# Performance work log

Hardware: AMD Instinct MI355X
Metric: run time of the kernel (lower is better)

The kernel has to match this reference:

```python
import jax, jax.numpy as jnp
import numpy as np

K = 6

def _diag_indices(H, W):
    # stable argsort of anti-diagonal index i+j over row-major flattening
    i = np.arange(H)[:, None]
    j = np.arange(W)[None, :]
    order = np.argsort((i + j).ravel(), kind='stable')
    return order, np.argsort(order, kind='stable')

def _selective_scan(u, delta, A, Bs, Cs, D, delta_bias):
    # u, delta: (B,K,D,L); A: (K,D,N); Bs,Cs: (B,K,N,L); D,delta_bias: (K,D)
    delta = jax.nn.softplus(delta + delta_bias[None, :, :, None])
    dA = jnp.exp(jnp.einsum('bkdl,kdn->lbkdn', delta, A))          # (L,B,K,D,N)
    dBu = jnp.einsum('bkdl,bknl,bkdl->lbkdn', delta, Bs, u)         # (L,B,K,D,N)
    Cl = jnp.moveaxis(Cs, -1, 0)                                    # (L,B,K,N)
    x0 = jnp.zeros(dA.shape[1:], dA.dtype)
    def step(x, inp):
        dA_t, dBu_t, C_t = inp
        x = dA_t * x + dBu_t
        y = jnp.einsum('bkdn,bkn->bkd', x, C_t)
        return x, y
    _, ys = jax.lax.scan(step, x0, (dA, dBu, Cl))
    y = jnp.moveaxis(ys, 0, -1)                                     # (B,K,D,L)
    return y + u * D[None, :, :, None]

def reference(x, W_in, conv_w, conv_b, x_proj_w, dt_w, dt_b, A_logs, Ds, ln_g, ln_b, W_out):
    B, H, W, C = x.shape
    L = H * W
    di = dt_w.shape[1]
    dt_rank = dt_w.shape[2]
    N = A_logs.shape[1]
    # in_proj (no bias) and split
    xz = jnp.einsum('bhwc,oc->bhwo', x, W_in)
    xx, z = jnp.split(xz, 2, axis=-1)
    # depthwise conv 3x3, SAME padding, + bias, SiLU
    xc = jnp.transpose(xx, (0, 3, 1, 2))                            # (B,di,H,W)
    xc = jax.lax.conv_general_dilated(xc, conv_w, (1, 1), 'SAME',
            feature_group_count=di, dimension_numbers=('NCHW', 'OIHW', 'NCHW'))
    xc = jax.nn.silu(xc + conv_b[None, :, None, None])
    # build 6 scan orderings
    x_flat = xc.reshape(B, di, L)
    x_t = jnp.transpose(xc, (0, 1, 3, 2)).reshape(B, di, L)
    x_hwwh = jnp.stack([x_flat, x_t], axis=1)                       # (B,2,di,L)
    xs4 = jnp.concatenate([x_hwwh, x_hwwh[..., ::-1]], axis=1)      # (B,4,di,L)
    x_invhh = jnp.flip(xc, axis=-1).reshape(B, di, L)               # flip W only
    x_hh = jnp.stack([x_flat, x_invhh], axis=1)                     # (B,2,di,L)
    diag_idx, rev_idx = _diag_indices(H, W)
    xs = jnp.concatenate([xs4, x_hh[..., diag_idx]], axis=1)        # (B,6,di,L)
    # projections
    x_dbl = jnp.einsum('bkdl,kcd->bkcl', xs, x_proj_w)
    dts, Bs, Cs = jnp.split(x_dbl, [dt_rank, dt_rank + N], axis=2)
    dts = jnp.einsum('bkrl,kdr->bkdl', dts, dt_w)
    A = -jnp.exp(A_logs).reshape(K, di, N)
    out_y = _selective_scan(xs, dts, A, Bs, Cs, Ds.reshape(K, di), dt_b)
    # undo the 6 orderings
    inv_y = out_y[:, 2:4][..., ::-1]
    wh_y = jnp.transpose(out_y[:, 1].reshape(B, di, W, H), (0, 1, 3, 2)).reshape(B, di, L)
    invwh_y = jnp.transpose(inv_y[:, 1].reshape(B, di, W, H), (0, 1, 3, 2)).reshape(B, di, L)
    transhh = out_y[:, 4:6][..., rev_idx]
    invhh = transhh[:, 1][..., ::-1]
    y = out_y[:, 0] + inv_y[:, 0] + wh_y + invwh_y + transhh[:, 0] + invhh  # (B,di,L)
    y = jnp.transpose(y, (0, 2, 1)).reshape(B, H, W, di)
    # LayerNorm (eps=1e-5)
    mu = y.mean(-1, keepdims=True)
    var = ((y - mu) ** 2).mean(-1, keepdims=True)
    y = (y - mu) * jax.lax.rsqrt(var + 1e-5) * ln_g + ln_b
    y = y * jax.nn.silu(z)
    return jnp.einsum('bhwd,od->bhwo', y, W_out)

def setup_inputs():
    key = jax.random.key(0)
    ks = jax.random.split(key, 8)
    d_model, di, N, dt_rank = 64, 128, 16, 4
    x = jax.random.normal(ks[0], (1, 64, 64, d_model), jnp.float32)
    W_in = jax.random.normal(ks[1], (2 * di, d_model), jnp.float32) * d_model ** -0.5
    conv_w = jax.random.normal(ks[2], (di, 1, 3, 3), jnp.float32) / 3.0
    conv_b = jnp.zeros((di,), jnp.float32)
    x_proj_w = jax.random.normal(ks[3], (K, dt_rank + 2 * N, di), jnp.float32) * di ** -0.5
    s = dt_rank ** -0.5
    dt_w = jax.random.uniform(ks[4], (K, di, dt_rank), jnp.float32, -s, s)
    dt = jnp.exp(jax.random.uniform(ks[5], (K, di), jnp.float32)
                 * (np.log(0.1) - np.log(0.001)) + np.log(0.001))
    dt = jnp.clip(dt, 1e-4)
    dt_b = dt + jnp.log(-jnp.expm1(-dt))
    A_logs = jnp.log(jnp.tile(jnp.arange(1, N + 1, dtype=jnp.float32)[None, :], (K * di, 1)))
    Ds = jnp.ones((K * di,), jnp.float32)
    ln_g = jnp.ones((di,), jnp.float32)
    ln_b = jnp.zeros((di,), jnp.float32)
    W_out = jax.random.normal(ks[6], (d_model, di), jnp.float32) * di ** -0.5
    return {"x": x, "W_in": W_in, "conv_w": conv_w, "conv_b": conv_b,
            "x_proj_w": x_proj_w, "dt_w": dt_w, "dt_b": dt_b, "A_logs": A_logs,
            "Ds": Ds, "ln_g": ln_g, "ln_b": ln_b, "W_out": W_out}
```

## Files before the change

kernel.cpp:

```cpp
#include <hip/hip_runtime.h>
#include <math.h>

#define L    4096
#define DI   128
#define NS   16
#define KK   6
#define DTR  4
#define CM   64
#define NC   256
#define CH   (L/NC)

__device__ __forceinline__ float softplus_f(float x){
    return x > 20.f ? x : __logf(1.f + __expf(x));
}
__device__ __forceinline__ float silu_f(float x){
    return x / (1.f + __expf(-x));
}

__device__ __forceinline__ int rankp(int p){
    int h = p >> 6, w = p & 63, s = h + w;
    int imin = s > 63 ? s - 63 : 0;
    int off = (s < 64) ? (s*(s+1))/2 : 4096 - ((127-s)*(128-s))/2;
    return off + (h - imin);
}

__device__ __forceinline__ int perm_in(int k, int l, const int* __restrict__ diag){
    switch(k){
        case 0: return l;
        case 1: return ((l&63)<<6) | (l>>6);
        case 2: return (L-1) - l;
        case 3: { int m = (L-1)-l; return ((m&63)<<6) | (m>>6); }
        case 4: return diag[l];
        default: return diag[l] ^ 63;
    }
}

__global__ void k_diag(int* __restrict__ diag_idx){
    int p = blockIdx.x*256 + threadIdx.x;
    if(p >= L) return;
    diag_idx[rankp(p)] = p;
}

__global__ __launch_bounds__(256) void k_inproj(const float* __restrict__ x,
                                                const float* __restrict__ W_in,
                                                float* __restrict__ xx_t,
                                                float* __restrict__ sz){
    int pb = blockIdx.x * 16;
    int o  = threadIdx.x;
    __shared__ float xr[16][CM];
    ((float4*)&xr[0][0])[o] = ((const float4*)(x + (size_t)pb*CM))[o];
    float4 w[16];
    const float4* wrow = (const float4*)(W_in + (size_t)o*CM);
    #pragma unroll
    for(int q=0;q<16;q++) w[q] = wrow[q];
    __syncthreads();
    #pragma unroll
    for(int pi=0; pi<16; pi++){
        float acc = 0.f;
        const float4* xv4 = (const float4*)&xr[pi][0];
        #pragma unroll
        for(int q=0;q<16;q++){
            float4 xv = xv4[q];
            acc += w[q].x*xv.x + w[q].y*xv.y + w[q].z*xv.z + w[q].w*xv.w;
        }
        int p = pb + pi;
        if(o < DI) xx_t[(size_t)p*DI + o] = acc;
        else       sz[(size_t)p*DI + (o-DI)] = silu_f(acc);
    }
}

__global__ __launch_bounds__(256) void k_conv(const float* __restrict__ xx_t,
                                              const float* __restrict__ cw,
                                              const float* __restrict__ cb,
                                              float* __restrict__ xc_t){
    int idx = blockIdx.x*256 + threadIdx.x;
    int d = idx & 127, p = idx >> 7;
    int h = p >> 6, w = p & 63;
    float acc = cb[d];
    #pragma unroll
    for(int dh=-1; dh<=1; dh++){
        int hh = h+dh; if(hh < 0 || hh >= 64) continue;
        #pragma unroll
        for(int dw=-1; dw<=1; dw++){
            int ww = w+dw; if(ww < 0 || ww >= 64) continue;
            acc += cw[d*9 + (dh+1)*3+(dw+1)] * xx_t[(size_t)(hh*64+ww)*DI + d];
        }
    }
    xc_t[idx] = silu_f(acc);
}

#define XT_S 132
__global__ __launch_bounds__(256) void k_proj(const float* __restrict__ xc_t,
                                              const float* __restrict__ xpw,
                                              const int* __restrict__ diag,
                                              float* __restrict__ dts,
                                              float* __restrict__ BT,
                                              float* __restrict__ CT){
    int k  = blockIdx.x >> 6;
    int l0 = (blockIdx.x & 63) * 64;
    int t  = threadIdx.x;
    __shared__ float xt[64*XT_S];
    #pragma unroll
    for(int q=0;q<8;q++){
        int lin = q*256 + t;
        int row = lin >> 5, col4 = lin & 31;
        int p = perm_in(k, l0+row, diag);
        float4 v = ((const float4*)(xc_t + (size_t)p*DI))[col4];
        *((float4*)(xt + row*XT_S + col4*4)) = v;
    }
    __syncthreads();
    int l = t & 63, c0 = (t>>6)*9;
    const float* xr = xt + l*XT_S;
    float acc[9];
    #pragma unroll
    for(int j=0;j<9;j++) acc[j] = 0.f;
    const float4* wbase = (const float4*)(xpw + (size_t)k*36*DI);
    for(int dd4=0; dd4<32; dd4++){
        float4 xv = *((const float4*)(xr + dd4*4));
        #pragma unroll
        for(int j=0;j<9;j++){
            float4 wv = wbase[(c0+j)*32 + dd4];
            acc[j] += wv.x*xv.x + wv.y*xv.y + wv.z*xv.z + wv.w*xv.w;
        }
    }
    #pragma unroll
    for(int j=0;j<9;j++){
        int c = c0 + j;
        if(c < 4)        dts[((size_t)k*4 + c)*L + l0 + l] = acc[j];
        else if(c < 20)  BT[((size_t)k*L + l0 + l)*NS + (c-4)]  = acc[j];
        else             CT[((size_t)k*L + l0 + l)*NS + (c-20)] = acc[j];
    }
}

__global__ __launch_bounds__(128) void k_scan1(const float* __restrict__ xc_t,
                                               const float* __restrict__ dts,
                                               const float* __restrict__ BT,
                                               const float* __restrict__ dtw,
                                               const float* __restrict__ dtb,
                                               const float* __restrict__ A_logs,
                                               const int* __restrict__ diag,
                                               float* __restrict__ apb,
                                               float* __restrict__ xlb){
    int bk = blockIdx.x;
    int k = bk >> 8, cc = bk & (NC-1);
    int d = threadIdx.x;
    int l0 = cc*CH;

    __shared__ float Bt[CH*NS];
    __shared__ float dtt[4*CH];
    __shared__ int   pt[CH];

    if(d < 64) ((float4*)Bt)[d] = ((const float4*)(BT + ((size_t)k*L + l0)*NS))[d];
    else { int j = d-64; int r = j>>4, i = j&15;
           dtt[j] = dts[((size_t)k*4 + r)*L + l0 + i]; }
    if(d < CH) pt[d] = perm_in(k, l0+d, diag);
    __syncthreads();

    float4 w4 = ((const float4*)dtw)[(size_t)k*DI + d];
    float  bb = dtb[k*DI + d];
    float A[NS];
    {
        const float4* ar = (const float4*)(A_logs + ((size_t)k*DI + d)*NS);
        #pragma unroll
        for(int q=0;q<4;q++){
            float4 a4 = ar[q];
            A[q*4+0] = -__expf(a4.x); A[q*4+1] = -__expf(a4.y);
            A[q*4+2] = -__expf(a4.z); A[q*4+3] = -__expf(a4.w);
        }
    }
    float x[NS], ap[NS];
    #pragma unroll
    for(int n=0;n<NS;n++){ x[n] = 0.f; ap[n] = 1.f; }

    float u_nxt = xc_t[(size_t)pt[0]*DI + d];
    #pragma unroll
    for(int i=0;i<CH;i++){
        float u = u_nxt;
        if(i+1 < CH) u_nxt = xc_t[(size_t)pt[i+1]*DI + d];
        float dv = bb + w4.x*dtt[i] + w4.y*dtt[CH+i] + w4.z*dtt[2*CH+i] + w4.w*dtt[3*CH+i];
        float delta = softplus_f(dv);
        float du = delta*u;
        const float* Bi = Bt + i*NS;
        #pragma unroll
        for(int n=0;n<NS;n++){
            float da = __expf(delta*A[n]);
            x[n] = da*x[n] + du*Bi[n];
            ap[n] *= da;
        }
    }
    float* apd = apb + ((size_t)bk*DI + d)*NS;
    float* xld = xlb + ((size_t)bk*DI + d)*NS;
    #pragma unroll
    for(int q=0;q<4;q++){
        ((float4*)apd)[q] = make_float4(ap[q*4],ap[q*4+1],ap[q*4+2],ap[q*4+3]);
        ((float4*)xld)[q] = make_float4(x[q*4], x[q*4+1], x[q*4+2], x[q*4+3]);
    }
}

__global__ __launch_bounds__(256) void k_comb(float* __restrict__ apb,
                                              const float* __restrict__ xlb){
    int tid = blockIdx.x*256 + threadIdx.x;
    int k = tid >> 11, rem = tid & 2047;
    size_t base = (size_t)k*NC*2048 + rem;
    float run = 0.f;
    float a[8], xl[8];
    #pragma unroll
    for(int q=0;q<8;q++){ a[q] = apb[base + (size_t)q*2048]; xl[q] = xlb[base + (size_t)q*2048]; }
    for(int b=0; b<NC/8; b++){
        float a2[8], x2[8];
        if(b+1 < NC/8){
            #pragma unroll
            for(int q=0;q<8;q++){
                size_t off = base + (size_t)((b+1)*8+q)*2048;
                a2[q] = apb[off]; x2[q] = xlb[off];
            }
        }
        #pragma unroll
        for(int q=0;q<8;q++){
            size_t off = base + (size_t)(b*8+q)*2048;
            apb[off] = run;
            run = a[q]*run + xl[q];
        }
        #pragma unroll
        for(int q=0;q<8;q++){ a[q] = a2[q]; xl[q] = x2[q]; }
    }
}

__global__ __launch_bounds__(128) void k_scan2(const float* __restrict__ xc_t,
                                               const float* __restrict__ dts,
                                               const float* __restrict__ BT,
                                               const float* __restrict__ CT,
                                               const float* __restrict__ dtw,
                                               const float* __restrict__ dtb,
                                               const float* __restrict__ A_logs,
                                               const float* __restrict__ Dsv,
                                               const int* __restrict__ diag,
                                               const float* __restrict__ inib,
                                               float* __restrict__ yk){
    int bk = blockIdx.x;
    int k = bk >> 8, cc = bk & (NC-1);
    int d = threadIdx.x;
    int l0 = cc*CH;

    __shared__ float Bt[CH*NS];
    __shared__ float Ct[CH*NS];
    __shared__ float dtt[4*CH];
    __shared__ int   pt[CH];

    if(d < 64){
        ((float4*)Bt)[d] = ((const float4*)(BT + ((size_t)k*L + l0)*NS))[d];
        int r = d>>4, i = d&15;
        dtt[d] = dts[((size_t)k*4 + r)*L + l0 + i];
    } else {
        ((float4*)Ct)[d-64] = ((const float4*)(CT + ((size_t)k*L + l0)*NS))[d-64];
    }
    if(d < CH) pt[d] = perm_in(k, l0+d, diag);
    __syncthreads();

    float4 w4 = ((const float4*)dtw)[(size_t)k*DI + d];
    float  bb = dtb[k*DI + d];
    float  Dv = Dsv[k*DI + d];
    float A[NS];
    {
        const float4* ar = (const float4*)(A_logs + ((size_t)k*DI + d)*NS);
        #pragma unroll
        for(int q=0;q<4;q++){
            float4 a4 = ar[q];
            A[q*4+0] = -__expf(a4.x); A[q*4+1] = -__expf(a4.y);
            A[q*4+2] = -__expf(a4.z); A[q*4+3] = -__expf(a4.w);
        }
    }
    float x[NS];
    {
        const float4* ir = (const float4*)(inib + ((size_t)bk*DI + d)*NS);
        #pragma unroll
        for(int q=0;q<4;q++){
            float4 v = ir[q];
            x[q*4+0]=v.x; x[q*4+1]=v.y; x[q*4+2]=v.z; x[q*4+3]=v.w;
        }
    }

    float u_nxt = xc_t[(size_t)pt[0]*DI + d];
    #pragma unroll
    for(int i=0;i<CH;i++){
        float u = u_nxt;
        if(i+1 < CH) u_nxt = xc_t[(size_t)pt[i+1]*DI + d];
        float dv = bb + w4.x*dtt[i] + w4.y*dtt[CH+i] + w4.z*dtt[2*CH+i] + w4.w*dtt[3*CH+i];
        float delta = softplus_f(dv);
        float du = delta*u;
        const float* Bi = Bt + i*NS;
        const float* Ci = Ct + i*NS;
        float y = 0.f;
        #pragma unroll
        for(int n=0;n<NS;n++){
            float da = __expf(delta*A[n]);
            x[n] = da*x[n] + du*Bi[n];
            y += x[n]*Ci[n];
        }
        yk[((size_t)k*L + l0 + i)*DI + d] = y + u*Dv;
    }
}

__global__ __launch_bounds__(128) void k_out(const float* __restrict__ yk,
                                             const float* __restrict__ sz,
                                             const float* __restrict__ ln_g,
                                             const float* __restrict__ ln_b,
                                             const float* __restrict__ W_out,
                                             float* __restrict__ out){
    int pb = blockIdx.x*8;
    int d = threadIdx.x;
    __shared__ float ms[8][DI];
    __shared__ float red[8][2][2];
    float g = ln_g[d], bc = ln_b[d];
    float yv[8];
    #pragma unroll
    for(int pi=0;pi<8;pi++){
        int p = pb+pi;
        int tp = ((p&63)<<6) | (p>>6);
        float y;
        y  = yk[((size_t)0*L + p)*DI + d];
        y += yk[((size_t)1*L + tp)*DI + d];
        y += yk[((size_t)2*L + (L-1-p))*DI + d];
        y += yk[((size_t)3*L + (L-1-tp))*DI + d];
        y += yk[((size_t)4*L + rankp(p))*DI + d];
        y += yk[((size_t)5*L + rankp(L-1-p))*DI + d];
        yv[pi] = y;
        float s1 = y, s2 = y*y;
        #pragma unroll
        for(int m=1;m<64;m<<=1){ s1 += __shfl_xor(s1,m,64); s2 += __shfl_xor(s2,m,64); }
        if((d&63)==0){ red[pi][d>>6][0] = s1; red[pi][d>>6][1] = s2; }
    }
    __syncthreads();
    #pragma unroll
    for(int pi=0;pi<8;pi++){
        float mu  = (red[pi][0][0]+red[pi][1][0]) * (1.f/DI);
        float var = (red[pi][0][1]+red[pi][1][1]) * (1.f/DI) - mu*mu;
        float yh = (yv[pi]-mu)*rsqrtf(var+1e-5f)*g + bc;
        ms[pi][d] = yh * sz[(size_t)(pb+pi)*DI + d];
    }
    __syncthreads();
    int o = d & 63, hf = d >> 6;
    float4 w[32];
    const float4* wr4 = (const float4*)(W_out + (size_t)o*DI);
    #pragma unroll
    for(int q=0;q<32;q++) w[q] = wr4[q];
    for(int pi=hf; pi<8; pi+=2){
        float acc = 0.f;
        const float4* mr = (const float4*)ms[pi];
        #pragma unroll
        for(int q=0;q<32;q++){
            float4 xv = mr[q];
            acc += w[q].x*xv.x + w[q].y*xv.y + w[q].z*xv.z + w[q].w*xv.w;
        }
        out[(size_t)(pb+pi)*CM + o] = acc;
    }
}

extern "C" void kernel_launch(void* const* d_in, const int* in_sizes, int n_in,
                              void* d_out, int out_size, void* d_ws, size_t ws_size,
                              hipStream_t stream) {
    const float* x      = (const float*)d_in[0];
    const float* W_in   = (const float*)d_in[1];
    const float* conv_w = (const float*)d_in[2];
    const float* conv_b = (const float*)d_in[3];
    const float* xpw    = (const float*)d_in[4];
    const float* dtw    = (const float*)d_in[5];
    const float* dtb    = (const float*)d_in[6];
    const float* A_logs = (const float*)d_in[7];
    const float* Dsv    = (const float*)d_in[8];
    const float* ln_g   = (const float*)d_in[9];
    const float* ln_b   = (const float*)d_in[10];
    const float* W_out  = (const float*)d_in[11];
    float* out = (float*)d_out;

    float* ws = (float*)d_ws;
    float* xx_t = ws;
    float* sz   = xx_t + (size_t)L*DI;
    float* xc_t = sz   + (size_t)L*DI;
    float* dts  = xc_t + (size_t)L*DI;
    float* BT   = dts  + (size_t)KK*4*L;
    float* CT   = BT   + (size_t)KK*L*NS;
    float* apb  = CT   + (size_t)KK*L*NS;
    float* xlb  = apb  + (size_t)KK*NC*DI*NS;
    float* yk   = xlb  + (size_t)KK*NC*DI*NS;
    int*   diag = (int*)(yk + (size_t)KK*L*DI);

    k_diag  <<<L/256, 256, 0, stream>>>(diag);
    k_inproj<<<L/16, 256, 0, stream>>>(x, W_in, xx_t, sz);
    k_conv  <<<(L*DI)/256, 256, 0, stream>>>(xx_t, conv_w, conv_b, xc_t);
    k_proj  <<<KK*64, 256, 0, stream>>>(xc_t, xpw, diag, dts, BT, CT);
    k_scan1 <<<KK*NC, 128, 0, stream>>>(xc_t, dts, BT, dtw, dtb, A_logs, diag, apb, xlb);
    k_comb  <<<KK*DI*NS/256, 256, 0, stream>>>(apb, xlb);
    k_scan2 <<<KK*NC, 128, 0, stream>>>(xc_t, dts, BT, CT, dtw, dtb, A_logs, Dsv, diag, apb, yk);
    k_out   <<<L/8, 128, 0, stream>>>(yk, sz, ln_g, ln_b, W_out, out);
}
```

Measured before the change: 195.1 us.

## Fuse pipeline into front kernel plus cooperative persistent scan kernel

Merges in_proj and the depthwise conv into one tiled kernel with halo recompute, and computes the diagonal permutation analytically instead of through a lookup table. The x_proj is fused into the first scan pass, which now emits a local y and cumulative delta. A correction pass adds the carried-in state as C·exp(A·S)·x0, so the second full recurrence over the chunk is no longer run. The remaining stages run in one cooperative persistent kernel with grid syncs, falling back to separate launches. This trades launch overhead and extra passes for grid-sync costs, larger workspace traffic and halo recomputation.

Measured after the change: 220.0 us. +12.8%, slower.

```diff
diff --git a/kernel.cpp b/kernel.cpp
--- a/kernel.cpp
+++ b/kernel.cpp
@@ -1,14 +1,18 @@
 #include <hip/hip_runtime.h>
+#include <hip/hip_cooperative_groups.h>
 #include <math.h>
+
+namespace cg = cooperative_groups;
 
 #define L    4096
 #define DI   128
 #define NS   16
 #define KK   6
-#define DTR  4
 #define CM   64
 #define NC   256
-#define CH   (L/NC)
+#define CH   16
+#define NU   (KK*NC)
+#define SHSZ 2688
 
 __device__ __forceinline__ float softplus_f(float x){
     return x > 20.f ? x : __logf(1.f + __expf(x));
@@ -23,141 +27,160 @@
     int off = (s < 64) ? (s*(s+1))/2 : 4096 - ((127-s)*(128-s))/2;
     return off + (h - imin);
 }
-
-__device__ __forceinline__ int perm_in(int k, int l, const int* __restrict__ diag){
+__device__ __forceinline__ int diag_pix(int l){
+    if(l < 2080){
+        int s = (int)((sqrtf(8.f*(float)l + 1.f) - 1.f)*0.5f);
+        if((s+1)*(s+2)/2 <= l) s++;
+        else if(s*(s+1)/2 > l) s--;
+        int t = l - s*(s+1)/2;
+        return t*64 + (s - t);
+    } else {
+        int r = 4096 - l;
+        int q = (int)((sqrtf(8.f*(float)r + 1.f) - 1.f)*0.5f);
+        if(q*(q+1)/2 < r) q++;
+        else if((q-1)*q/2 >= r) q--;
+        int s = 127 - q;
+        int off = 4096 - q*(q+1)/2;
+        int t = l - off;
+        int h = (s - 63) + t;
+        return h*64 + (s - h);
+    }
+}
+__device__ __forceinline__ int perm_in(int k, int l){
     switch(k){
         case 0: return l;
         case 1: return ((l&63)<<6) | (l>>6);
         case 2: return (L-1) - l;
         case 3: { int m = (L-1)-l; return ((m&63)<<6) | (m>>6); }
-        case 4: return diag[l];
-        default: return diag[l] ^ 63;
-    }
-}
-
-__global__ void k_diag(int* __restrict__ diag_idx){
-    int p = blockIdx.x*256 + threadIdx.x;
-    if(p >= L) return;
-    diag_idx[rankp(p)] = p;
-}
-
-__global__ __launch_bounds__(256) void k_inproj(const float* __restrict__ x,
-                                                const float* __restrict__ W_in,
-                                                float* __restrict__ xx_t,
-                                                float* __restrict__ sz){
-    int pb = blockIdx.x * 16;
-    int o  = threadIdx.x;
-    __shared__ float xr[16][CM];
-    ((float4*)&xr[0][0])[o] = ((const float4*)(x + (size_t)pb*CM))[o];
+        case 4: return diag_pix(l);
+        default: return diag_pix(l) ^ 63;
+    }
+}
+
+__global__ __launch_bounds__(256) void k_front(const float* __restrict__ x,
+                                               const float* __restrict__ W_in,
+                                               const float* __restrict__ cw,
+                                               const float* __restrict__ cb,
+                                               float* __restrict__ xc_t,
+                                               float* __restrict__ sz){
+    int ty = blockIdx.x >> 4, tx = blockIdx.x & 15;
+    int h0 = ty*4, w0 = tx*4;
+    int t = threadIdx.x;
+    __shared__ float xr[36*CM];
+    __shared__ float xxs[36*DI];
+
+    for(int lin = t; lin < 36*16; lin += 256){
+        int px = lin >> 4, c4 = lin & 15;
+        int hh = h0 - 1 + px/6, ww = w0 - 1 + px%6;
+        float4 v = make_float4(0.f,0.f,0.f,0.f);
+        if(hh >= 0 && hh < 64 && ww >= 0 && ww < 64)
+            v = ((const float4*)(x + (size_t)(hh*64+ww)*CM))[c4];
+        *((float4*)(xr + px*CM + c4*4)) = v;
+    }
+    __syncthreads();
+
+    int o = t;
     float4 w[16];
     const float4* wrow = (const float4*)(W_in + (size_t)o*CM);
     #pragma unroll
     for(int q=0;q<16;q++) w[q] = wrow[q];
-    __syncthreads();
-    #pragma unroll
-    for(int pi=0; pi<16; pi++){
+    for(int px=0; px<36; px++){
+        const float4* xv4 = (const float4*)(xr + px*CM);
         float acc = 0.f;
-        const float4* xv4 = (const float4*)&xr[pi][0];
         #pragma unroll
         for(int q=0;q<16;q++){
             float4 xv = xv4[q];
             acc += w[q].x*xv.x + w[q].y*xv.y + w[q].z*xv.z + w[q].w*xv.w;
         }
-        int p = pb + pi;
-        if(o < DI) xx_t[(size_t)p*DI + o] = acc;
-        else       sz[(size_t)p*DI + (o-DI)] = silu_f(acc);
-    }
-}
-
-__global__ __launch_bounds__(256) void k_conv(const float* __restrict__ xx_t,
-                                              const float* __restrict__ cw,
-                                              const float* __restrict__ cb,
-                                              float* __restrict__ xc_t){
-    int idx = blockIdx.x*256 + threadIdx.x;
-    int d = idx & 127, p = idx >> 7;
-    int h = p >> 6, w = p & 63;
-    float acc = cb[d];
-    #pragma unroll
-    for(int dh=-1; dh<=1; dh++){
-        int hh = h+dh; if(hh < 0 || hh >= 64) continue;
-        #pragma unroll
-        for(int dw=-1; dw<=1; dw++){
-            int ww = w+dw; if(ww < 0 || ww >= 64) continue;
-            acc += cw[d*9 + (dh+1)*3+(dw+1)] * xx_t[(size_t)(hh*64+ww)*DI + d];
-        }
-    }
-    xc_t[idx] = silu_f(acc);
-}
-
-#define XT_S 132
-__global__ __launch_bounds__(256) void k_proj(const float* __restrict__ xc_t,
-                                              const float* __restrict__ xpw,
-                                              const int* __restrict__ diag,
-                                              float* __restrict__ dts,
-                                              float* __restrict__ BT,
-                                              float* __restrict__ CT){
-    int k  = blockIdx.x >> 6;
-    int l0 = (blockIdx.x & 63) * 64;
-    int t  = threadIdx.x;
-    __shared__ float xt[64*XT_S];
-    #pragma unroll
-    for(int q=0;q<8;q++){
-        int lin = q*256 + t;
-        int row = lin >> 5, col4 = lin & 31;
-        int p = perm_in(k, l0+row, diag);
-        float4 v = ((const float4*)(xc_t + (size_t)p*DI))[col4];
-        *((float4*)(xt + row*XT_S + col4*4)) = v;
-    }
-    __syncthreads();
-    int l = t & 63, c0 = (t>>6)*9;
-    const float* xr = xt + l*XT_S;
-    float acc[9];
-    #pragma unroll
-    for(int j=0;j<9;j++) acc[j] = 0.f;
-    const float4* wbase = (const float4*)(xpw + (size_t)k*36*DI);
-    for(int dd4=0; dd4<32; dd4++){
-        float4 xv = *((const float4*)(xr + dd4*4));
-        #pragma unroll
-        for(int j=0;j<9;j++){
-            float4 wv = wbase[(c0+j)*32 + dd4];
-            acc[j] += wv.x*xv.x + wv.y*xv.y + wv.z*xv.z + wv.w*xv.w;
-        }
-    }
-    #pragma unroll
-    for(int j=0;j<9;j++){
-        int c = c0 + j;
-        if(c < 4)        dts[((size_t)k*4 + c)*L + l0 + l] = acc[j];
-        else if(c < 20)  BT[((size_t)k*L + l0 + l)*NS + (c-4)]  = acc[j];
-        else             CT[((size_t)k*L + l0 + l)*NS + (c-20)] = acc[j];
-    }
-}
-
-__global__ __launch_bounds__(128) void k_scan1(const float* __restrict__ xc_t,
-                                               const float* __restrict__ dts,
-                                               const float* __restrict__ BT,
-                                               const float* __restrict__ dtw,
-                                               const float* __restrict__ dtb,
-                                               const float* __restrict__ A_logs,
-                                               const int* __restrict__ diag,
-                                               float* __restrict__ apb,
-                                               float* __restrict__ xlb){
-    int bk = blockIdx.x;
-    int k = bk >> 8, cc = bk & (NC-1);
-    int d = threadIdx.x;
+        if(o < DI) xxs[px*DI + o] = acc;
+        else {
+            int hr = px/6, wc = px%6;
+            if(hr >= 1 && hr <= 4 && wc >= 1 && wc <= 4){
+                int pg = (h0 + hr - 1)*64 + (w0 + wc - 1);
+                sz[(size_t)pg*DI + (o-DI)] = silu_f(acc);
+            }
+        }
+    }
+    __syncthreads();
+
+    int d = t & 127, ph = t >> 7;
+    float cwr[9];
+    #pragma unroll
+    for(int j=0;j<9;j++) cwr[j] = cw[d*9+j];
+    float cbd = cb[d];
+    #pragma unroll
+    for(int i=0;i<8;i++){
+        int idx = ph*8 + i;
+        int r = idx >> 2, c = idx & 3;
+        float acc = cbd;
+        #pragma unroll
+        for(int dh=0; dh<3; dh++)
+            #pragma unroll
+            for(int dw=0; dw<3; dw++)
+                acc += cwr[dh*3+dw] * xxs[((r+dh)*6 + (c+dw))*DI + d];
+        int pg = (h0+r)*64 + (w0+c);
+        xc_t[(size_t)pg*DI + d] = silu_f(acc);
+    }
+}
+
+__device__ __forceinline__ void dev_PA(int u, int t, float* shm,
+        const float* __restrict__ xc_t, const float* __restrict__ xpw,
+        const float* __restrict__ dtw, const float* __restrict__ dtb,
+        const float* __restrict__ A_logs, const float* __restrict__ Dsv,
+        float* __restrict__ apb, float* __restrict__ xlb,
+        float* __restrict__ Srb, float* __restrict__ CTb, float* __restrict__ yk)
+{
+    int k = u >> 8, cc = u & 255;
     int l0 = cc*CH;
-
-    __shared__ float Bt[CH*NS];
-    __shared__ float dtt[4*CH];
-    __shared__ int   pt[CH];
-
-    if(d < 64) ((float4*)Bt)[d] = ((const float4*)(BT + ((size_t)k*L + l0)*NS))[d];
-    else { int j = d-64; int r = j>>4, i = j&15;
-           dtt[j] = dts[((size_t)k*4 + r)*L + l0 + i]; }
-    if(d < CH) pt[d] = perm_in(k, l0+d, diag);
-    __syncthreads();
-
+    float* xt  = shm;
+    float* Bt  = shm + 2112;
+    float* Ct  = shm + 2368;
+    float* dtt = shm + 2624;
+    __syncthreads();
+    #pragma unroll
+    for(int q=0;q<4;q++){
+        int lin = q*128 + t;
+        int row = lin >> 5, c4 = lin & 31;
+        int p = perm_in(k, l0 + row);
+        float4 v = ((const float4*)(xc_t + (size_t)p*DI))[c4];
+        *((float4*)(xt + row*132 + c4*4)) = v;
+    }
+    __syncthreads();
+    {
+        int lrow = t >> 3, c8 = t & 7;
+        const float4* xrow = (const float4*)(xt + lrow*132);
+        const float4* wb = (const float4*)(xpw + (size_t)k*36*DI);
+        int c4r = (c8 < 4) ? (32+c8) : 32;
+        float a0=0,a1=0,a2=0,a3=0,a4=0;
+        for(int dd4=0; dd4<32; dd4++){
+            float4 xv = xrow[dd4];
+            float4 w0 = wb[(c8    )*32 + dd4];
+            float4 w1 = wb[(8 +c8 )*32 + dd4];
+            float4 w2 = wb[(16+c8 )*32 + dd4];
+            float4 w3 = wb[(24+c8 )*32 + dd4];
+            float4 w4v= wb[(c4r   )*32 + dd4];
+            a0 += w0.x*xv.x + w0.y*xv.y + w0.z*xv.z + w0.w*xv.w;
+            a1 += w1.x*xv.x + w1.y*xv.y + w1.z*xv.z + w1.w*xv.w;
+            a2 += w2.x*xv.x + w2.y*xv.y + w2.z*xv.z + w2.w*xv.w;
+            a3 += w3.x*xv.x + w3.y*xv.y + w3.z*xv.z + w3.w*xv.w;
+            a4 += w4v.x*xv.x + w4v.y*xv.y + w4v.z*xv.z + w4v.w*xv.w;
+        }
+        if(c8 < 4) dtt[c8*16 + lrow] = a0;
+        else       Bt[lrow*16 + (c8-4)] = a0;
+        Bt[lrow*16 + 4 + c8] = a1;
+        if(c8 < 4) Bt[lrow*16 + 12 + c8] = a2;
+        else       Ct[lrow*16 + (c8-4)] = a2;
+        Ct[lrow*16 + 4 + c8] = a3;
+        if(c8 < 4) Ct[lrow*16 + 12 + c8] = a4;
+    }
+    __syncthreads();
+    CTb[(size_t)u*256 + t]       = Ct[t];
+    CTb[(size_t)u*256 + 128 + t] = Ct[128 + t];
+
+    int d = t;
     float4 w4 = ((const float4*)dtw)[(size_t)k*DI + d];
     float  bb = dtb[k*DI + d];
+    float  Dv = Dsv[k*DI + d];
     float A[NS];
     {
         const float4* ar = (const float4*)(A_logs + ((size_t)k*DI + d)*NS);
@@ -168,40 +191,44 @@
             A[q*4+2] = -__expf(a4.z); A[q*4+3] = -__expf(a4.w);
         }
     }
-    float x[NS], ap[NS];
-    #pragma unroll
-    for(int n=0;n<NS;n++){ x[n] = 0.f; ap[n] = 1.f; }
-
-    float u_nxt = xc_t[(size_t)pt[0]*DI + d];
+    float xs[NS];
+    float S = 0.f;
+    #pragma unroll
+    for(int n=0;n<NS;n++) xs[n] = 0.f;
     #pragma unroll
     for(int i=0;i<CH;i++){
-        float u = u_nxt;
-        if(i+1 < CH) u_nxt = xc_t[(size_t)pt[i+1]*DI + d];
-        float dv = bb + w4.x*dtt[i] + w4.y*dtt[CH+i] + w4.z*dtt[2*CH+i] + w4.w*dtt[3*CH+i];
+        float dv = bb + w4.x*dtt[i] + w4.y*dtt[16+i] + w4.z*dtt[32+i] + w4.w*dtt[48+i];
         float delta = softplus_f(dv);
-        float du = delta*u;
+        S += delta;
+        Srb[(size_t)u*2048 + i*128 + d] = S;
+        float uu = xt[i*132 + d];
+        float du = delta*uu;
+        float yv = uu*Dv;
         const float* Bi = Bt + i*NS;
+        const float* Ci = Ct + i*NS;
         #pragma unroll
         for(int n=0;n<NS;n++){
             float da = __expf(delta*A[n]);
-            x[n] = da*x[n] + du*Bi[n];
-            ap[n] *= da;
-        }
-    }
-    float* apd = apb + ((size_t)bk*DI + d)*NS;
-    float* xld = xlb + ((size_t)bk*DI + d)*NS;
+            xs[n] = da*xs[n] + du*Bi[n];
+            yv += xs[n]*Ci[n];
+        }
+        yk[(size_t)u*2048 + i*128 + d] = yv;
+    }
+    float* apd = apb + ((size_t)u*DI + d)*NS;
+    float* xld = xlb + ((size_t)u*DI + d)*NS;
     #pragma unroll
     for(int q=0;q<4;q++){
-        ((float4*)apd)[q] = make_float4(ap[q*4],ap[q*4+1],ap[q*4+2],ap[q*4+3]);
-        ((float4*)xld)[q] = make_float4(x[q*4], x[q*4+1], x[q*4+2], x[q*4+3]);
-    }
-}
-
-__global__ __launch_bounds__(256) void k_comb(float* __restrict__ apb,
-                                              const float* __restrict__ xlb){
-    int tid = blockIdx.x*256 + threadIdx.x;
-    int k = tid >> 11, rem = tid & 2047;
-    size_t base = (size_t)k*NC*2048 + rem;
+        ((float4*)apd)[q] = make_float4(__expf(A[q*4]*S), __expf(A[q*4+1]*S),
+                                        __expf(A[q*4+2]*S), __expf(A[q*4+3]*S));
+        ((float4*)xld)[q] = make_float4(xs[q*4],xs[q*4+1],xs[q*4+2],xs[q*4+3]);
+    }
+}
+
+__device__ __forceinline__ void dev_B(int tid, float* __restrict__ apb,
+                                      const float* __restrict__ xlb)
+{
+    int k2 = tid >> 11, rem = tid & 2047;
+    size_t base = (size_t)k2*NC*2048 + rem;
     float run = 0.f;
     float a[8], xl[8];
     #pragma unroll
@@ -226,134 +253,149 @@
     }
 }
 
-__global__ __launch_bounds__(128) void k_scan2(const float* __restrict__ xc_t,
-                                               const float* __restrict__ dts,
-                                               const float* __restrict__ BT,
-                                               const float* __restrict__ CT,
-                                               const float* __restrict__ dtw,
-                                               const float* __restrict__ dtb,
-                                               const float* __restrict__ A_logs,
-                                               const float* __restrict__ Dsv,
-                                               const int* __restrict__ diag,
-                                               const float* __restrict__ inib,
-                                               float* __restrict__ yk){
-    int bk = blockIdx.x;
-    int k = bk >> 8, cc = bk & (NC-1);
-    int d = threadIdx.x;
-    int l0 = cc*CH;
-
-    __shared__ float Bt[CH*NS];
-    __shared__ float Ct[CH*NS];
-    __shared__ float dtt[4*CH];
-    __shared__ int   pt[CH];
-
-    if(d < 64){
-        ((float4*)Bt)[d] = ((const float4*)(BT + ((size_t)k*L + l0)*NS))[d];
-        int r = d>>4, i = d&15;
-        dtt[d] = dts[((size_t)k*4 + r)*L + l0 + i];
-    } else {
-        ((float4*)Ct)[d-64] = ((const float4*)(CT + ((size_t)k*L + l0)*NS))[d-64];
-    }
-    if(d < CH) pt[d] = perm_in(k, l0+d, diag);
-    __syncthreads();
-
-    float4 w4 = ((const float4*)dtw)[(size_t)k*DI + d];
-    float  bb = dtb[k*DI + d];
-    float  Dv = Dsv[k*DI + d];
-    float A[NS];
+__device__ __forceinline__ void dev_C(int u, int t, float* shm,
+        const float* __restrict__ apb, const float* __restrict__ A_logs,
+        const float* __restrict__ Srb, const float* __restrict__ CTb,
+        float* __restrict__ yk)
+{
+    int k = u >> 8;
+    int d = t;
+    __syncthreads();
+    shm[t]       = CTb[(size_t)u*256 + t];
+    shm[128 + t] = CTb[(size_t)u*256 + 128 + t];
+    __syncthreads();
+    float xi[NS], A[NS];
     {
+        const float4* ir = (const float4*)(apb + ((size_t)u*DI + d)*NS);
         const float4* ar = (const float4*)(A_logs + ((size_t)k*DI + d)*NS);
         #pragma unroll
         for(int q=0;q<4;q++){
+            float4 v = ir[q];
+            xi[q*4]=v.x; xi[q*4+1]=v.y; xi[q*4+2]=v.z; xi[q*4+3]=v.w;
             float4 a4 = ar[q];
             A[q*4+0] = -__expf(a4.x); A[q*4+1] = -__expf(a4.y);
             A[q*4+2] = -__expf(a4.z); A[q*4+3] = -__expf(a4.w);
         }
     }
-    float x[NS];
+    #pragma unroll
+    for(int i=0;i<CH;i++){
+        size_t off = (size_t)u*2048 + i*128 + d;
+        float Sr = Srb[off];
+        const float* Ci = shm + i*NS;
+        float corr = 0.f;
+        #pragma unroll
+        for(int n=0;n<NS;n++) corr += Ci[n]*__expf(A[n]*Sr)*xi[n];
+        yk[off] += corr;
+    }
+}
+
+__device__ __forceinline__ void dev_D(int tile, int t, float* shm,
+        const float* __restrict__ yk, const float* __restrict__ sz,
+        const float* __restrict__ ln_g, const float* __restrict__ ln_b,
+        const float* __restrict__ W_out, float* __restrict__ out)
+{
+    float* ms  = shm;
+    float* po  = shm + 128;
+    float* red = shm + 256;
+    int o = t & 63, half = t >> 6;
+    float4 wo[16];
+    const float4* wr4 = (const float4*)(W_out + (size_t)o*DI + half*64);
+    #pragma unroll
+    for(int q=0;q<16;q++) wo[q] = wr4[q];
+    float g = ln_g[t], bc = ln_b[t];
+
+    int p0 = tile*4;
+    #pragma unroll
+    for(int px=0; px<4; px++){
+        int pg = p0 + px;
+        int tp = ((pg&63)<<6) | (pg>>6);
+        float y;
+        y  = yk[((size_t)0*L + pg)*DI + t];
+        y += yk[((size_t)1*L + tp)*DI + t];
+        y += yk[((size_t)2*L + (L-1-pg))*DI + t];
+        y += yk[((size_t)3*L + (L-1-tp))*DI + t];
+        y += yk[((size_t)4*L + rankp(pg))*DI + t];
+        y += yk[((size_t)5*L + rankp(L-1-pg))*DI + t];
+        float s1 = y, s2 = y*y;
+        #pragma unroll
+        for(int m=1;m<64;m<<=1){ s1 += __shfl_xor(s1,m,64); s2 += __shfl_xor(s2,m,64); }
+        __syncthreads();
+        if((t&63)==0){ red[(t>>6)*2] = s1; red[(t>>6)*2+1] = s2; }
+        __syncthreads();
+        float mu  = (red[0]+red[2]) * (1.f/DI);
+        float var = (red[1]+red[3]) * (1.f/DI) - mu*mu;
+        float yh = (y-mu)*rsqrtf(var+1e-5f)*g + bc;
+        ms[t] = yh * sz[(size_t)pg*DI + t];
+        __syncthreads();
+        float acc = 0.f;
+        const float4* mr = (const float4*)(ms + half*64);
+        #pragma unroll
+        for(int q=0;q<16;q++){
+            float4 xv = mr[q];
+            acc += wo[q].x*xv.x + wo[q].y*xv.y + wo[q].z*xv.z + wo[q].w*xv.w;
+        }
+        po[half*64 + o] = acc;
+        __syncthreads();
+        if(t < 64) out[(size_t)pg*CM + t] = po[t] + po[64+t];
+    }
+}
+
+__global__ __launch_bounds__(128) void k_coop(const float* __restrict__ xc_t,
+                                              const float* __restrict__ sz,
+                                              const float* __restrict__ xpw,
+                                              const float* __restrict__ dtw,
+                                              const float* __restrict__ dtb,
+                                              const float* __restrict__ A_logs,
+                                              const float* __restrict__ Dsv,
+                                              const float* __restrict__ ln_g,
+                                              const float* __restrict__ ln_b,
+                                              const float* __restrict__ W_out,
+                                              float* __restrict__ apb,
+                                              float* __restrict__ xlb,
+                                              float* __restrict__ Srb,
+                                              float* __restrict__ CTb,
+                                              float* __restrict__ yk,
+                                              float* __restrict__ out){
+    cg::grid_group grid = cg::this_grid();
+    __shared__ float shm[SHSZ];
+    int t = threadIdx.x;
+    for(int u = blockIdx.x; u < NU; u += gridDim.x)
+        dev_PA(u, t, shm, xc_t, xpw, dtw, dtb, A_logs, Dsv, apb, xlb, Srb, CTb, yk);
+    grid.sync();
     {
-        const float4* ir = (const float4*)(inib + ((size_t)bk*DI + d)*NS);
-        #pragma unroll
-        for(int q=0;q<4;q++){
-            float4 v = ir[q];
-            x[q*4+0]=v.x; x[q*4+1]=v.y; x[q*4+2]=v.z; x[q*4+3]=v.w;
-        }
-    }
-
-    float u_nxt = xc_t[(size_t)pt[0]*DI + d];
-    #pragma unroll
-    for(int i=0;i<CH;i++){
-        float u = u_nxt;
-        if(i+1 < CH) u_nxt = xc_t[(size_t)pt[i+1]*DI + d];
-        float dv = bb + w4.x*dtt[i] + w4.y*dtt[CH+i] + w4.z*dtt[2*CH+i] + w4.w*dtt[3*CH+i];
-        float delta = softplus_f(dv);
-        float du = delta*u;
-        const float* Bi = Bt + i*NS;
-        const float* Ci = Ct + i*NS;
-        float y = 0.f;
-        #pragma unroll
-        for(int n=0;n<NS;n++){
-            float da = __expf(delta*A[n]);
-            x[n] = da*x[n] + du*Bi[n];
-            y += x[n]*Ci[n];
-        }
-        yk[((size_t)k*L + l0 + i)*DI + d] = y + u*Dv;
-    }
-}
-
-__global__ __launch_bounds__(128) void k_out(const float* __restrict__ yk,
-                                             const float* __restrict__ sz,
-                                             const float* __restrict__ ln_g,
-                                             const float* __restrict__ ln_b,
-                                             const float* __restrict__ W_out,
-                                             float* __restrict__ out){
-    int pb = blockIdx.x*8;
-    int d = threadIdx.x;
-    __shared__ float ms[8][DI];
-    __shared__ float red[8][2][2];
-    float g = ln_g[d], bc = ln_b[d];
-    float yv[8];
-    #pragma unroll
-    for(int pi=0;pi<8;pi++){
-        int p = pb+pi;
-        int tp = ((p&63)<<6) | (p>>6);
-        float y;
-        y  = yk[((size_t)0*L + p)*DI + d];
-        y += yk[((size_t)1*L + tp)*DI + d];
-        y += yk[((size_t)2*L + (L-1-p))*DI + d];
-        y += yk[((size_t)3*L + (L-1-tp))*DI + d];
-        y += yk[((size_t)4*L + rankp(p))*DI + d];
-        y += yk[((size_t)5*L + rankp(L-1-p))*DI + d];
-        yv[pi] = y;
-        float s1 = y, s2 = y*y;
-        #pragma unroll
-        for(int m=1;m<64;m<<=1){ s1 += __shfl_xor(s1,m,64); s2 += __shfl_xor(s2,m,64); }
-        if((d&63)==0){ red[pi][d>>6][0] = s1; red[pi][d>>6][1] = s2; }
-    }
-    __syncthreads();
-    #pragma unroll
-    for(int pi=0;pi<8;pi++){
-        float mu  = (red[pi][0][0]+red[pi][1][0]) * (1.f/DI);
-        float var = (red[pi][0][1]+red[pi][1][1]) * (1.f/DI) - mu*mu;
-        float yh = (yv[pi]-mu)*rsqrtf(var+1e-5f)*g + bc;
-        ms[pi][d] = yh * sz[(size_t)(pb+pi)*DI + d];
-    }
-    __syncthreads();
-    int o = d & 63, hf = d >> 6;
-    float4 w[32];
-    const float4* wr4 = (const float4*)(W_out + (size_t)o*DI);
-    #pragma unroll
-    for(int q=0;q<32;q++) w[q] = wr4[q];
-    for(int pi=hf; pi<8; pi+=2){
-        float acc = 0.f;
-        const float4* mr = (const float4*)ms[pi];
-        #pragma unroll
-        for(int q=0;q<32;q++){
-            float4 xv = mr[q];
-            acc += w[q].x*xv.x + w[q].y*xv.y + w[q].z*xv.z + w[q].w*xv.w;
-        }
-        out[(size_t)(pb+pi)*CM + o] = acc;
-    }
+        int tid = blockIdx.x*128 + t;
+        if(tid < KK*DI*NS) dev_B(tid, apb, xlb);
+    }
+    grid.sync();
+    for(int u = blockIdx.x; u < NU; u += gridDim.x)
+        dev_C(u, t, shm, apb, A_logs, Srb, CTb, yk);
+    grid.sync();
+    for(int tile = blockIdx.x; tile < L/4; tile += gridDim.x)
+        dev_D(tile, t, shm, yk, sz, ln_g, ln_b, W_out, out);
+}
+
+__global__ __launch_bounds__(128) void k_PA(const float* xc_t, const float* xpw,
+        const float* dtw, const float* dtb, const float* A_logs, const float* Dsv,
+        float* apb, float* xlb, float* Srb, float* CTb, float* yk){
+    __shared__ float shm[SHSZ];
+    for(int u = blockIdx.x; u < NU; u += gridDim.x)
+        dev_PA(u, threadIdx.x, shm, xc_t, xpw, dtw, dtb, A_logs, Dsv, apb, xlb, Srb, CTb, yk);
+}
+__global__ __launch_bounds__(128) void k_B(float* apb, const float* xlb){
+    int tid = blockIdx.x*128 + threadIdx.x;
+    if(tid < KK*DI*NS) dev_B(tid, apb, xlb);
+}
+__global__ __launch_bounds__(128) void k_C(const float* apb, const float* A_logs,
+        const float* Srb, const float* CTb, float* yk){
+    __shared__ float shm[256];
+    for(int u = blockIdx.x; u < NU; u += gridDim.x)
+        dev_C(u, threadIdx.x, shm, apb, A_logs, Srb, CTb, yk);
+}
+__global__ __launch_bounds__(128) void k_D(const float* yk, const float* sz,
+        const float* ln_g, const float* ln_b, const float* W_out, float* out){
+    __shared__ float shm[260];
+    for(int tile = blockIdx.x; tile < L/4; tile += gridDim.x)
+        dev_D(tile, threadIdx.x, shm, yk, sz, ln_g, ln_b, W_out, out);
 }
 
 extern "C" void kernel_launch(void* const* d_in, const int* in_sizes, int n_in,
@@ -374,23 +416,38 @@
     float* out = (float*)d_out;
 
     float* ws = (float*)d_ws;
-    float* xx_t = ws;
-    float* sz   = xx_t + (size_t)L*DI;
-    float* xc_t = sz   + (size_t)L*DI;
-    float* dts  = xc_t + (size_t)L*DI;
-    float* BT   = dts  + (size_t)KK*4*L;
-    float* CT   = BT   + (size_t)KK*L*NS;
-    float* apb  = CT   + (size_t)KK*L*NS;
-    float* xlb  = apb  + (size_t)KK*NC*DI*NS;
-    float* yk   = xlb  + (size_t)KK*NC*DI*NS;
-    int*   diag = (int*)(yk + (size_t)KK*L*DI);
-
-    k_diag  <<<L/256, 256, 0, stream>>>(diag);
-    k_inproj<<<L/16, 256, 0, stream>>>(x, W_in, xx_t, sz);
-    k_conv  <<<(L*DI)/256, 256, 0, stream>>>(xx_t, conv_w, conv_b, xc_t);
-    k_proj  <<<KK*64, 256, 0, stream>>>(xc_t, xpw, diag, dts, BT, CT);
-    k_scan1 <<<KK*NC, 128, 0, stream>>>(xc_t, dts, BT, dtw, dtb, A_logs, diag, apb, xlb);
-    k_comb  <<<KK*DI*NS/256, 256, 0, stream>>>(apb, xlb);
-    k_scan2 <<<KK*NC, 128, 0, stream>>>(xc_t, dts, BT, CT, dtw, dtb, A_logs, Dsv, diag, apb, yk);
-    k_out   <<<L/8, 128, 0, stream>>>(yk, sz, ln_g, ln_b, W_out, out);
-}
+    float* xc_t = ws;
+    float* sz   = xc_t + (size_t)L*DI;
+    float* apb  = sz   + (size_t)L*DI;
+    float* xlb  = apb  + (size_t)NU*DI*NS;
+    float* Srb  = xlb  + (size_t)NU*DI*NS;
+    float* yk   = Srb  + (size_t)NU*2048;
+    float* CTb  = yk   + (size_t)KK*L*DI;
+
+    k_front<<<256, 256, 0, stream>>>(x, W_in, conv_w, conv_b, xc_t, sz);
+
+    int coop_ok = 0;
+    hipDeviceGetAttribute(&coop_ok, hipDeviceAttributeCooperativeLaunch, 0);
+    int nb = 0;
+    if(coop_ok)
+        hipOccupancyMaxActiveBlocksPerMultiprocessor(&nb, k_coop, 128, 0);
+    int grid = nb * 256;
+    if(grid > NU) grid = NU;
+
+    bool done = false;
+    if(coop_ok && grid >= 256){
+        void* args[] = {(void*)&xc_t, (void*)&sz, (void*)&xpw, (void*)&dtw, (void*)&dtb,
+                        (void*)&A_logs, (void*)&Dsv, (void*)&ln_g, (void*)&ln_b,
+                        (void*)&W_out, (void*)&apb, (void*)&xlb, (void*)&Srb,
+                        (void*)&CTb, (void*)&yk, (void*)&out};
+        hipError_t e = hipLaunchCooperativeKernel((void*)k_coop, dim3(grid), dim3(128),
+                                                  args, 0, stream);
+        done = (e == hipSuccess);
+    }
+    if(!done){
+        k_PA<<<NU, 128, 0, stream>>>(xc_t, xpw, dtw, dtb, A_logs, Dsv, apb, xlb, Srb, CTb, yk);
+        k_B <<<KK*DI*NS/128, 128, 0, stream>>>(apb, xlb);
+        k_C <<<NU, 128, 0, stream>>>(apb, A_logs, Srb, CTb, yk);
+        k_D <<<L/4, 128, 0, stream>>>(yk, sz, ln_g, ln_b, W_out, out);
+    }
+}
```
